# Optimization experiments

Hardware: AMD Instinct MI355X
Metric: run time of the kernel (lower is better)

Reference implementation:

```python
import jax, jax.numpy as jnp
from jax import lax
import numpy as np

B, C, H, W = 8, 256, 64, 64
STRIDE, NH = 2, 8
ED_QK, ED_V = 64, 256  # embed_dim//ratio (divisible by heads), embed_dim
HQ, WQ = H // STRIDE, W // STRIDE
L = HQ * WQ


def conv2d(x, w, b, stride=1, pad=0):
    y = lax.conv_general_dilated(x, w, (stride, stride), ((pad, pad), (pad, pad)),
                                 dimension_numbers=('NCHW', 'OIHW', 'NCHW'))
    return y + b[None, :, None, None]


def setup_inputs() -> dict:
    key = jax.random.key(0)
    ks = jax.random.split(key, 24)
    s = 0.05
    f32 = jnp.float32
    inp = {
        'qkv_pos': jax.random.normal(ks[0], (B, C, H, W), f32),
        'qkv_cha': jax.random.normal(ks[1], (B, C, H, W), f32),
        # POS branch params (standard convs)
        'Wq_pos': jax.random.normal(ks[2], (ED_QK, C, 2, 2), f32) * s,
        'bq_pos': jax.random.normal(ks[3], (ED_QK,), f32) * s,
        'Wk_pos': jax.random.normal(ks[4], (ED_QK, C, 2, 2), f32) * s,
        'bk_pos': jax.random.normal(ks[5], (ED_QK,), f32) * s,
        'Wv_pos': jax.random.normal(ks[6], (ED_V, C, 2, 2), f32) * s,
        'bv_pos': jax.random.normal(ks[7], (ED_V,), f32) * s,
        'Wo_pos': jax.random.normal(ks[8], (C, ED_V, 3, 3), f32) * s,
        'bo_pos': jax.random.normal(ks[9], (C,), f32) * s,
        'gamma_pos': jnp.full((1,), 0.5, f32),
        # CHA branch params (grouped convs, groups=C, 1 in-ch -> NH out-ch per group)
        'Wq_cha': jax.random.normal(ks[10], (C, NH, 2, 2), f32) * s,
        'bq_cha': jax.random.normal(ks[11], (C, NH), f32) * s,
        'Wk_cha': jax.random.normal(ks[12], (C, NH, 2, 2), f32) * s,
        'bk_cha': jax.random.normal(ks[13], (C, NH), f32) * s,
        'Wv_cha': jax.random.normal(ks[14], (C, NH, 2, 2), f32) * s,
        'bv_cha': jax.random.normal(ks[15], (C, NH), f32) * s,
        # grouped ConvTranspose2d (groups=C, NH in-ch per group -> 1 out-ch), k=s=2
        'Wt_cha': jax.random.normal(ks[16], (C, NH, 2, 2), f32) * s,
        'bt_cha': jax.random.normal(ks[17], (C,), f32) * s,
        'gamma_cha': jnp.full((1,), 0.5, f32),
        # fusion conv: concat -> 2C in, C out, 3x3
        'Wf': jax.random.normal(ks[18], (C, 2 * C, 3, 3), f32) * s,
        'bf': jax.random.normal(ks[19], (C,), f32) * s,
    }
    return inp


def _gproj(x, w, b):
    # grouped conv with kernel==stride==2, 1 in-ch per group -> NH out-ch per group
    xp = x.reshape(B, C, HQ, STRIDE, WQ, STRIDE)
    y = jnp.einsum('bgikjl,ghkl->bghij', xp, w) + b[None, :, :, None, None]
    # channel order c = g*NH + h (torch grouped-conv layout); torch then reshapes
    # the flat C*NH channels into (NH, C) -> same as a direct reshape here
    return y.reshape(B, NH, C, L)


def reference(qkv_pos, qkv_cha, Wq_pos, bq_pos, Wk_pos, bk_pos, Wv_pos, bv_pos,
              Wo_pos, bo_pos, gamma_pos, Wq_cha, bq_cha, Wk_cha, bk_cha,
              Wv_cha, bv_cha, Wt_cha, bt_cha, gamma_cha, Wf, bf):
    hd = ED_QK // NH
    # ---- POS (spatial) attention ----
    qp = conv2d(qkv_pos, Wq_pos, bq_pos, STRIDE).reshape(B, NH, hd, L).transpose(0, 1, 3, 2)
    kp = conv2d(qkv_pos, Wk_pos, bk_pos, STRIDE).reshape(B, NH, hd, L).transpose(0, 1, 3, 2)
    vp = conv2d(qkv_pos, Wv_pos, bv_pos, STRIDE).reshape(B, NH, ED_V // NH, L).transpose(0, 1, 3, 2)
    attn_p = jax.nn.softmax(jnp.einsum('bhqd,bhkd->bhqk', qp, kp) * (hd ** -0.5), axis=-1)
    op = jnp.einsum('bhqk,bhkd->bhqd', attn_p, vp).transpose(0, 1, 3, 2).reshape(B, ED_V, HQ, WQ)
    op = conv2d(op, Wo_pos, bo_pos, 1, 1)
    op = jax.image.resize(op, (B, C, H, W), 'bilinear')  # Upsample(align_corners=False)
    out_pos = qkv_pos + op * gamma_pos
    # ---- CHA (channel) attention ----
    qc = _gproj(qkv_cha, Wq_cha, bq_cha)  # [B,NH,C,L]
    kc = _gproj(qkv_cha, Wk_cha, bk_cha)
    vc = _gproj(qkv_cha, Wv_cha, bv_cha)
    attn_c = jax.nn.softmax(jnp.einsum('bhcl,bhdl->bhcd', qc, kc) * (L ** -0.5), axis=-1)
    oc = jnp.einsum('bhcd,bhdl->bhcl', attn_c, vc)  # [B,NH,C,L]
    # flat channel c = h*C + g; grouped ConvTranspose2d groups by c//NH -> reshape (C,NH)
    ocg = oc.reshape(B, C, NH, HQ, WQ)
    oc = jnp.einsum('bgipq,gikl->bgpkql', ocg, Wt_cha).reshape(B, C, H, W) + bt_cha[None, :, None, None]
    out_cha = qkv_cha + oc * gamma_cha
    # ---- fusion: concat (slices are full since slides=0) + 3x3 conv ----
    out = jnp.concatenate([out_pos, out_cha], axis=1)
    return conv2d(out, Wf, bf, 1, 1)
```

## Files before the change

### kernel.cpp

```cpp
#include <hip/hip_runtime.h>
#include <math.h>


typedef __attribute__((ext_vector_type(8))) short bf16x8;
typedef __attribute__((ext_vector_type(4))) float f32x4;

__device__ __forceinline__ ushort f2bf(float f) {
  union { float f; unsigned u; } v; v.f = f;
  unsigned r = (v.u + 0x7FFFu + ((v.u >> 16) & 1u)) >> 16;
  return (ushort)r;
}

__global__ __launch_bounds__(256) void k_prep_all(
    const float* __restrict__ Wf, const float* __restrict__ Wo,
    const float* __restrict__ Wq, const float* __restrict__ Wk,
    const float* __restrict__ Wv,
    ushort* __restrict__ Wpf9, ushort* __restrict__ Wpo9,
    ushort* __restrict__ Wqkvp)
{
  const int i = blockIdx.x * 256 + threadIdx.x;
  if (i < 1179648) {
    const int t = i / 131072;
    const int r = i - t * 131072;
    const int oc = r >> 9, c = r & 511;
    Wpf9[i] = f2bf(Wf[((size_t)oc * 512 + c) * 9 + t]);
  } else if (i < 1179648 + 589824) {
    const int j = i - 1179648;
    const int t = j / 65536;
    const int r = j - t * 65536;
    const int oc = r >> 8, c = r & 255;
    Wpo9[j] = f2bf(Wo[((size_t)oc * 256 + c) * 9 + t]);
  } else {
    const int j = i - 1769472;
    const int o = j >> 10, k = j & 1023;
    float v;
    if (o < 64)       v = Wq[(size_t)o * 1024 + k];
    else if (o < 128) v = Wk[(size_t)(o - 64) * 1024 + k];
    else              v = Wv[(size_t)(o - 128) * 1024 + k];
    Wqkvp[j] = f2bf(v);
  }
}

__global__ __launch_bounds__(256) void k_zero_init(
    ushort* __restrict__ fused, ushort* __restrict__ op_pad,
    ushort* __restrict__ Qb)
{
  const int t = blockIdx.x * 256 + threadIdx.x;
  uint4 z = {0u, 0u, 0u, 0u};
  if (t < 133120) {
    const int e = t & 63;
    const int pi = (t >> 6) % 260;
    const int b = t / 16640;
    int y, x;
    if (pi < 66)       { y = 0;            x = pi; }
    else if (pi < 132) { y = 65;           x = pi - 66; }
    else if (pi < 196) { y = pi - 132 + 1; x = 0; }
    else               { y = pi - 196 + 1; x = 65; }
    *(uint4*)(fused + ((size_t)b * 4356 + y * 66 + x) * 512 + e * 8) = z;
  } else if (t < 133120 + 33792) {
    const int j = t - 133120;
    const int e = j & 31;
    const int pi = (j >> 5) % 132;
    const int b = j / 4224;
    int y, x;
    if (pi < 34)       { y = 0;            x = pi; }
    else if (pi < 68)  { y = 33;           x = pi - 34; }
    else if (pi < 100) { y = pi - 68 + 1;  x = 0; }
    else               { y = pi - 100 + 1; x = 33; }
    *(uint4*)(op_pad + ((size_t)b * 1156 + y * 34 + x) * 256 + e * 8) = z;
  } else {
    const int j = t - 166912;
    *(uint4*)(Qb + (size_t)j * 8) = z;
  }
}

__global__ __launch_bounds__(256) void k_pack_pos(
    const float* __restrict__ x, ushort* __restrict__ Ap)
{
  const int t = blockIdx.x * 256 + threadIdx.x;
  const int j4 = t & 7;
  const int i  = (t >> 3) & 31;
  const int c  = (t >> 8) & 255;
  const int b  = t >> 16;
  const float* xb = x + (((size_t)b * 256 + c) << 12) + (2 * i) * 64 + 8 * j4;
  union { float4 v[2]; float f[8]; } r0, r1;
  r0.v[0] = *(const float4*)(xb);
  r0.v[1] = *(const float4*)(xb + 4);
  r1.v[0] = *(const float4*)(xb + 64);
  r1.v[1] = *(const float4*)(xb + 68);
  #pragma unroll
  for (int jj = 0; jj < 4; ++jj) {
    const int l = i * 32 + j4 * 4 + jj;
    union { ushort u[4]; uint2 d; } pk;
    pk.u[0] = f2bf(r0.f[2 * jj]);
    pk.u[1] = f2bf(r0.f[2 * jj + 1]);
    pk.u[2] = f2bf(r1.f[2 * jj]);
    pk.u[3] = f2bf(r1.f[2 * jj + 1]);
    *(uint2*)(Ap + ((((size_t)b << 10) + l) << 10) + c * 4) = pk.d;
  }
}

__global__ __launch_bounds__(256) void k_pos_qkv_mfma(
    const ushort* __restrict__ Ap, const ushort* __restrict__ Wqkv,
    const float* __restrict__ bq, const float* __restrict__ bk,
    const float* __restrict__ bv,
    ushort* __restrict__ Qb, ushort* __restrict__ Kb, ushort* __restrict__ Vtb)
{
  const int n0 = blockIdx.x * 128, oc0 = blockIdx.y * 128, b = blockIdx.z;
  const int tid = threadIdx.x, lane = tid & 63, w = tid >> 6;
  __shared__ ushort As[128][32], Bs[128][32];
  const ushort* Abw = Wqkv + (size_t)oc0 * 1024;
  const ushort* Bb  = Ap + (((size_t)b << 10) + n0) * 1024;
  const int wr = w >> 1, wc = w & 1;
  f32x4 acc[4][4];
  #pragma unroll
  for (int mi = 0; mi < 4; ++mi)
    #pragma unroll
    for (int ni = 0; ni < 4; ++ni) {
      f32x4 z = {0.f, 0.f, 0.f, 0.f};
      acc[mi][ni] = z;
    }
  for (int kc = 0; kc < 1024; kc += 32) {
    __syncthreads();
    #pragma unroll
    for (int q = 0; q < 2; ++q) {
      int idx = w * 128 + q * 64 + lane;
      int row = idx >> 2, seg = idx & 3;
      const ushort* srcA = Abw + (size_t)row * 1024 + kc + seg * 8;
      const ushort* srcB = Bb + (size_t)row * 1024 + kc + seg * 8;
      char* dstA = (char*)&As[0][0] + w * 2048 + q * 1024;
      char* dstB = (char*)&Bs[0][0] + w * 2048 + q * 1024;
      __builtin_amdgcn_global_load_lds(
          (const __attribute__((address_space(1))) unsigned*)srcA,
          (__attribute__((address_space(3))) unsigned*)dstA, 16, 0, 0);
      __builtin_amdgcn_global_load_lds(
          (const __attribute__((address_space(1))) unsigned*)srcB,
          (__attribute__((address_space(3))) unsigned*)dstB, 16, 0, 0);
    }
    __syncthreads();
    bf16x8 af[4], bfv[4];
    #pragma unroll
    for (int mi = 0; mi < 4; ++mi)
      af[mi] = *(const bf16x8*)&As[wr * 64 + mi * 16 + (lane & 15)][(lane >> 4) * 8];
    #pragma unroll
    for (int ni = 0; ni < 4; ++ni)
      bfv[ni] = *(const bf16x8*)&Bs[wc * 64 + ni * 16 + (lane & 15)][(lane >> 4) * 8];
    #pragma unroll
    for (int mi = 0; mi < 4; ++mi)
      #pragma unroll
      for (int ni = 0; ni < 4; ++ni)
        acc[mi][ni] = __builtin_amdgcn_mfma_f32_16x16x32_bf16(
            af[mi], bfv[ni], acc[mi][ni], 0, 0, 0);
  }
  #pragma unroll
  for (int mi = 0; mi < 4; ++mi) {
    const int oc = oc0 + wr * 64 + mi * 16 + (lane >> 4) * 4;
    if (oc >= 384) continue;
    if (oc < 64) {
      const int hh = oc >> 3, e = oc & 7;
      float4 bb = *(const float4*)(bq + oc);
      #pragma unroll
      for (int ni = 0; ni < 4; ++ni) {
        const int l = n0 + wc * 64 + ni * 16 + (lane & 15);
        union { ushort u[4]; uint2 d; } pk;
        pk.u[0] = f2bf((acc[mi][ni][0] + bb.x) * 0.35355339059327373f);
        pk.u[1] = f2bf((acc[mi][ni][1] + bb.y) * 0.35355339059327373f);
        pk.u[2] = f2bf((acc[mi][ni][2] + bb.z) * 0.35355339059327373f);
        pk.u[3] = f2bf((acc[mi][ni][3] + bb.w) * 0.35355339059327373f);
        *(uint2*)(Qb + (((((size_t)b * 8 + hh) << 10) + l) << 5) + e) = pk.d;
      }
    } else if (oc < 128) {
      const int o2 = oc - 64, hh = o2 >> 3, e = o2 & 7;
      float4 bb = *(const float4*)(bk + o2);
      #pragma unroll
      for (int ni = 0; ni < 4; ++ni) {
        const int l = n0 + wc * 64 + ni * 16 + (lane & 15);
        union { ushort u[4]; uint2 d; } pk;
        pk.u[0] = f2bf(acc[mi][ni][0] + bb.x);
        pk.u[1] = f2bf(acc[mi][ni][1] + bb.y);
        pk.u[2] = f2bf(acc[mi][ni][2] + bb.z);
        pk.u[3] = f2bf(acc[mi][ni][3] + bb.w);
        *(uint2*)(Kb + (((((size_t)b * 8 + hh) << 10) + l) << 5) + e) = pk.d;
      }
    } else {
      const int o2 = oc - 128, hh = o2 >> 5, dd = o2 & 31;
      float4 bb = *(const float4*)(bv + o2);
      #pragma unroll
      for (int ni = 0; ni < 4; ++ni) {
        const int l = n0 + wc * 64 + ni * 16 + (lane & 15);
        ushort* vb = Vtb + ((((size_t)b * 8 + hh) * 32 + dd) << 10) + l;
        vb[0]      = f2bf(acc[mi][ni][0] + bb.x);
        vb[1024]   = f2bf(acc[mi][ni][1] + bb.y);
        vb[2048]   = f2bf(acc[mi][ni][2] + bb.z);
        vb[3072]   = f2bf(acc[mi][ni][3] + bb.w);
      }
    }
  }
}

__global__ __launch_bounds__(256) void k_pos_flash(
    const ushort* __restrict__ Qb, const ushort* __restrict__ Kb,
    const ushort* __restrict__ Vtb, ushort* __restrict__ op_pad)
{
  const int qt = blockIdx.x, h = blockIdx.y, b = blockIdx.z;
  const int bh = b * 8 + h;
  const int tid = threadIdx.x, lane = tid & 63, wq = tid >> 6;
  const int c = lane & 15, g = lane >> 4;
  __shared__ __align__(16) ushort Ps[4][32][72];
  const int qbase = qt * 128 + wq * 32;
  bf16x8 qf[2];
  #pragma unroll
  for (int nt = 0; nt < 2; ++nt)
    qf[nt] = *(const bf16x8*)(Qb + (((size_t)bh << 10) + qbase + nt * 16 + c) * 32 + g * 8);
  f32x4 o[2][2];
  #pragma unroll
  for (int mt = 0; mt < 2; ++mt)
    #pragma unroll
    for (int nt = 0; nt < 2; ++nt) {
      f32x4 z = {0.f, 0.f, 0.f, 0.f};
      o[mt][nt] = z;
    }
  float m[2] = {-1e30f, -1e30f}, l[2] = {0.f, 0.f};
  const ushort* Kbh = Kb + ((size_t)bh << 15);
  const ushort* Vbh = Vtb + ((size_t)bh << 15);

  for (int kt = 0; kt < 16; ++kt) {
    const int kb0 = kt * 64;
    bf16x8 kf[4];
    #pragma unroll
    for (int mt = 0; mt < 4; ++mt)
      kf[mt] = *(const bf16x8*)(Kbh + (size_t)(kb0 + mt * 16 + c) * 32 + g * 8);
    f32x4 s[4][2];
    #pragma unroll
    for (int mt = 0; mt < 4; ++mt)
      #pragma unroll
      for (int nt = 0; nt < 2; ++nt) {
        f32x4 z = {0.f, 0.f, 0.f, 0.f};
        s[mt][nt] = __builtin_amdgcn_mfma_f32_16x16x32_bf16(kf[mt], qf[nt], z, 0, 0, 0);
      }
    #pragma unroll
    for (int nt = 0; nt < 2; ++nt) {
      float tmax = -1e30f;
      #pragma unroll
      for (int mt = 0; mt < 4; ++mt)
        #pragma unroll
        for (int r = 0; r < 4; ++r)
          tmax = fmaxf(tmax, s[mt][nt][r]);
      tmax = fmaxf(tmax, __shfl_xor(tmax, 16, 64));
      tmax = fmaxf(tmax, __shfl_xor(tmax, 32, 64));
      const float mn = fmaxf(m[nt], tmax);
      const float alpha = __expf(m[nt] - mn);
      m[nt] = mn;
      float rs = 0.f;
      #pragma unroll
      for (int mt = 0; mt < 4; ++mt) {
        union { ushort u[4]; uint2 d; } pk;
        #pragma unroll
        for (int r = 0; r < 4; ++r) {
          float p = __expf(s[mt][nt][r] - mn);
          rs += p;
          pk.u[r] = f2bf(p);
        }
        *(uint2*)&Ps[wq][nt * 16 + c][mt * 16 + g * 4] = pk.d;
      }
      rs += __shfl_xor(rs, 16, 64);
      rs += __shfl_xor(rs, 32, 64);
      l[nt] = l[nt] * alpha + rs;
      #pragma unroll
      for (int mt = 0; mt < 2; ++mt)
        #pragma unroll
        for (int r = 0; r < 4; ++r)
          o[mt][nt][r] *= alpha;
    }
    #pragma unroll
    for (int kc = 0; kc < 2; ++kc) {
      bf16x8 vf[2], pf[2];
      #pragma unroll
      for (int mt = 0; mt < 2; ++mt)
        vf[mt] = *(const bf16x8*)(Vbh + (size_t)(mt * 16 + c) * 1024 + kb0 + kc * 32 + g * 8);
      #pragma unroll
      for (int nt = 0; nt < 2; ++nt)
        pf[nt] = *(const bf16x8*)&Ps[wq][nt * 16 + c][kc * 32 + g * 8];
      #pragma unroll
      for (int mt = 0; mt < 2; ++mt)
        #pragma unroll
        for (int nt = 0; nt < 2; ++nt)
          o[mt][nt] = __builtin_amdgcn_mfma_f32_16x16x32_bf16(vf[mt], pf[nt], o[mt][nt], 0, 0, 0);
    }
  }
  #pragma unroll
  for (int nt = 0; nt < 2; ++nt) {
    const float linv = 1.f / l[nt];
    const int q = qbase + nt * 16 + c;
    const int y = q >> 5, x = q & 31;
    ushort* dst = op_pad + ((size_t)b * 1156 + (y + 1) * 34 + (x + 1)) * 256 + h * 32;
    #pragma unroll
    for (int mt = 0; mt < 2; ++mt) {
      union { ushort u[4]; uint2 d; } pk;
      #pragma unroll
      for (int r = 0; r < 4; ++r)
        pk.u[r] = f2bf(o[mt][nt][r] * linv);
      *(uint2*)(dst + mt * 16 + g * 4) = pk.d;
    }
  }
}

template <int CIN, int S, int PW, int OUT_NHWC, int BN>
__global__ __launch_bounds__(256) void k_conv9_mfma(
    const ushort* __restrict__ in, const ushort* __restrict__ W9,
    const float* __restrict__ bias, float* __restrict__ out)
{
  constexpr int BQ = BN / 64;
  constexpr int NI = BN / 32;
  const int n0 = blockIdx.x * BN, oc0 = blockIdx.y * 128, b = blockIdx.z;
  const int tid = threadIdx.x, lane = tid & 63, w = tid >> 6;
  __shared__ ushort As[128][32], Bs[BN][32];
  const int wr = w >> 1, wc = w & 1;
  f32x4 acc[4][NI];
  #pragma unroll
  for (int mi = 0; mi < 4; ++mi)
    #pragma unroll
    for (int ni = 0; ni < NI; ++ni) {
      f32x4 z = {0.f, 0.f, 0.f, 0.f};
      acc[mi][ni] = z;
    }
  int rowqA[2], segqA[2];
  #pragma unroll
  for (int q = 0; q < 2; ++q) {
    int idx = w * 128 + q * 64 + lane;
    rowqA[q] = idx >> 2;
    segqA[q] = (idx & 3) * 8;
  }
  int rowqB[BQ], segqB[BQ], basep[BQ];
  #pragma unroll
  for (int q = 0; q < BQ; ++q) {
    int idx = (BQ == 2) ? (w * 128 + q * 64 + lane) : tid;
    rowqB[q] = idx >> 2;
    segqB[q] = (idx & 3) * 8;
    int n = n0 + rowqB[q];
    int y = n / S, x = n % S;
    basep[q] = y * PW + x;
  }
  const ushort* inb = in + (size_t)b * (PW * PW) * CIN;

  for (int t = 0; t < 9; ++t) {
    const int offp = (t / 3) * PW + (t % 3);
    const ushort* wt = W9 + (size_t)t * 256 * CIN;
    for (int kc = 0; kc < CIN; kc += 32) {
      __syncthreads();
      #pragma unroll
      for (int q = 0; q < 2; ++q) {
        const ushort* srcA = wt + (size_t)(oc0 + rowqA[q]) * CIN + kc + segqA[q];
        char* dstA = (char*)&As[0][0] + w * 2048 + q * 1024;
        __builtin_amdgcn_global_load_lds(
            (const __attribute__((address_space(1))) unsigned*)srcA,
            (__attribute__((address_space(3))) unsigned*)dstA, 16, 0, 0);
      }
      #pragma unroll
      for (int q = 0; q < BQ; ++q) {
        const ushort* srcB = inb + (size_t)(basep[q] + offp) * CIN + kc + segqB[q];
        char* dstB = (char*)&Bs[0][0] + w * (BQ * 1024) + q * 1024;
        __builtin_amdgcn_global_load_lds(
            (const __attribute__((address_space(1))) unsigned*)srcB,
            (__attribute__((address_space(3))) unsigned*)dstB, 16, 0, 0);
      }
      __syncthreads();
      bf16x8 af[4], bfv[NI];
      #pragma unroll
      for (int mi = 0; mi < 4; ++mi)
        af[mi] = *(const bf16x8*)&As[wr * 64 + mi * 16 + (lane & 15)][(lane >> 4) * 8];
      #pragma unroll
      for (int ni = 0; ni < NI; ++ni)
        bfv[ni] = *(const bf16x8*)&Bs[wc * (BN / 2) + ni * 16 + (lane & 15)][(lane >> 4) * 8];
      #pragma unroll
      for (int mi = 0; mi < 4; ++mi)
        #pragma unroll
        for (int ni = 0; ni < NI; ++ni)
          acc[mi][ni] = __builtin_amdgcn_mfma_f32_16x16x32_bf16(
              af[mi], bfv[ni], acc[mi][ni], 0, 0, 0);
    }
  }
  if (OUT_NHWC) {
    float* outb = out + (size_t)b * (S * S) * 256;
    #pragma unroll
    for (int mi = 0; mi < 4; ++mi) {
      const int oc = oc0 + wr * 64 + mi * 16 + (lane >> 4) * 4;
      float4 bb = *(const float4*)(bias + oc);
      #pragma unroll
      for (int ni = 0; ni < NI; ++ni) {
        const int n = n0 + wc * (BN / 2) + ni * 16 + (lane & 15);
        float4 v;
        v.x = acc[mi][ni][0] + bb.x;
        v.y = acc[mi][ni][1] + bb.y;
        v.z = acc[mi][ni][2] + bb.z;
        v.w = acc[mi][ni][3] + bb.w;
        *(float4*)(outb + (size_t)n * 256 + oc) = v;
      }
    }
  } else {
    float* outb = out + (size_t)b * 256 * (S * S);
    #pragma unroll
    for (int mi = 0; mi < 4; ++mi) {
      #pragma unroll
      for (int r = 0; r < 4; ++r) {
        int oc = oc0 + wr * 64 + mi * 16 + (lane >> 4) * 4 + r;
        float bb = bias[oc];
        #pragma unroll
        for (int ni = 0; ni < NI; ++ni) {
          int n = n0 + wc * (BN / 2) + ni * 16 + (lane & 15);
          outb[(size_t)oc * (S * S) + n] = acc[mi][ni][r] + bb;
        }
      }
    }
  }
}

#define STAGE_CONV(s_, bi_)                                                    \
  {                                                                            \
    const int t_ = (s_) >> 3, kc_ = ((s_) & 7) << 6;                           \
    const ushort* wt_ = W9 + t_ * 131072 + kc_;                                \
    const ushort* ib_ = inb + ((t_ / 3) * 66 + (t_ % 3)) * 512 + kc_;          \
    _Pragma("unroll")                                                          \
    for (int q_ = 0; q_ < 2; ++q_) {                                           \
      __builtin_amdgcn_global_load_lds(                                        \
          (const __attribute__((address_space(1))) unsigned*)(wt_ + aInv[q_]), \
          (__attribute__((address_space(3))) unsigned*)                        \
              ((char*)lds + (bi_) * 16384 + (w * 16 + q_ * 8) * 128),          \
          16, 0, 0);                                                           \
    }                                                                          \
    _Pragma("unroll")                                                          \
    for (int q_ = 0; q_ < 4; ++q_) {                                           \
      __builtin_amdgcn_global_load_lds(                                        \
          (const __attribute__((address_space(1))) unsigned*)(ib_ + bInv[q_]), \
          (__attribute__((address_space(3))) unsigned*)                        \
              ((char*)lds + 49152 + (bi_) * 32768 + (w * 32 + q_ * 8) * 128),  \
          16, 0, 0);                                                           \
    }                                                                          \
  }

#define READ_FRAGS(rb_, AF_, BF_)                                              \
  {                                                                            \
    const ushort* As_ = lds + (rb_) * 8192 + (wm * 64 + c) * 64;               \
    const ushort* Bs_ = lds + 24576 + (rb_) * 16384 + (wn * 64 + c) * 64;      \
    _Pragma("unroll")                                                          \
    for (int mi_ = 0; mi_ < 4; ++mi_) {                                        \
      AF_[mi_][0] = *(const bf16x8*)(As_ + mi_ * 1024 + okh0);                 \
      AF_[mi_][1] = *(const bf16x8*)(As_ + mi_ * 1024 + okh1);                 \
    }                                                                          \
    _Pragma("unroll")                                                          \
    for (int ni_ = 0; ni_ < 4; ++ni_) {                                        \
      BF_[ni_][0] = *(const bf16x8*)(Bs_ + ni_ * 1024 + okh0);                 \
      BF_[ni_][1] = *(const bf16x8*)(Bs_ + ni_ * 1024 + okh1);                 \
    }                                                                          \
  }

#define MFMA_SET(AF_, BF_)                                                     \
  {                                                                            \
    __builtin_amdgcn_s_setprio(1);                                             \
    _Pragma("unroll")                                                          \
    for (int mi_ = 0; mi_ < 4; ++mi_)                                          \
      _Pragma("unroll")                                                        \
      for (int ni_ = 0; ni_ < 4; ++ni_) {                                      \
        acc[mi_][ni_] = __builtin_amdgcn_mfma_f32_16x16x32_bf16(               \
            AF_[mi_][0], BF_[ni_][0], acc[mi_][ni_], 0, 0, 0);                 \
        acc[mi_][ni_] = __builtin_amdgcn_mfma_f32_16x16x32_bf16(               \
            AF_[mi_][1], BF_[ni_][1], acc[mi_][ni_], 0, 0, 0);                 \
      }                                                                        \
    __builtin_amdgcn_s_setprio(0);                                             \
  }

#define PHASE_END(vm_)                                                         \
  {                                                                            \
    asm volatile("s_waitcnt lgkmcnt(0)" ::: "memory");                         \
    asm volatile("s_waitcnt vmcnt(" #vm_ ")" ::: "memory");                    \
    __builtin_amdgcn_sched_barrier(0);                                         \
    __builtin_amdgcn_s_barrier();                                              \
  }

__global__ __launch_bounds__(512, 2) void k_conv9_pipe(
    const ushort* __restrict__ in, const ushort* __restrict__ W9,
    const float* __restrict__ bias, float* __restrict__ out)
{
  const int n0 = blockIdx.x * 256, oc0 = blockIdx.y * 128, b = blockIdx.z;
  const int tid = threadIdx.x, lane = tid & 63, w = tid >> 6;
  const int wm = w >> 2, wn = w & 3;
  const int g = lane >> 4, c = lane & 15;
  __shared__ __align__(16) ushort lds[73728];
  const ushort* inb = in + (size_t)b * 4356 * 512;

  const int l8 = lane >> 3, lx = lane & 7;
  int aInv[2], bInv[4];
  #pragma unroll
  for (int q = 0; q < 2; ++q) {
    const int row = w * 16 + q * 8 + l8;
    const int cx = (((lx << 4) ^ ((row & 7) << 4)) >> 1);
    aInv[q] = (oc0 + row) * 512 + cx;
  }
  #pragma unroll
  for (int q = 0; q < 4; ++q) {
    const int row = w * 32 + q * 8 + l8;
    const int n = n0 + row;
    const int y = n >> 6, x = n & 63;
    const int cx = (((lx << 4) ^ ((row & 7) << 4)) >> 1);
    bInv[q] = (y * 66 + x) * 512 + cx;
  }

  const int sx = (c & 7) << 3;
  const int okh0 = (g * 8) ^ sx;
  const int okh1 = (32 + g * 8) ^ sx;

  f32x4 acc[4][4];
  #pragma unroll
  for (int mi = 0; mi < 4; ++mi)
    #pragma unroll
    for (int ni = 0; ni < 4; ++ni) {
      f32x4 z = {0.f, 0.f, 0.f, 0.f};
      acc[mi][ni] = z;
    }

  bf16x8 afE[4][2], bfE[4][2], afO[4][2], bfO[4][2];

  STAGE_CONV(0, 0);
  STAGE_CONV(1, 1);
  STAGE_CONV(2, 2);
  asm volatile("s_waitcnt vmcnt(12)" ::: "memory");
  __builtin_amdgcn_sched_barrier(0);
  __builtin_amdgcn_s_barrier();
  READ_FRAGS(0, afE, bfE);
  PHASE_END(6);

  int rb = 1;
  for (int p = 0; p < 68; p += 2) {
    READ_FRAGS(rb, afO, bfO);
    { int sb = rb + 2; if (sb >= 3) sb -= 3; STAGE_CONV(p + 3, sb); }
    MFMA_SET(afE, bfE);
    PHASE_END(6);
    ++rb; if (rb == 3) rb = 0;
    READ_FRAGS(rb, afE, bfE);
    { int sb = rb + 2; if (sb >= 3) sb -= 3; STAGE_CONV(p + 4, sb); }
    MFMA_SET(afO, bfO);
    PHASE_END(6);
    ++rb; if (rb == 3) rb = 0;
  }
  READ_FRAGS(rb, afO, bfO);
  { int sb = rb + 2; if (sb >= 3) sb -= 3; STAGE_CONV(71, sb); }
  MFMA_SET(afE, bfE);
  PHASE_END(6);
  ++rb; if (rb == 3) rb = 0;
  READ_FRAGS(rb, afE, bfE);
  MFMA_SET(afO, bfO);
  PHASE_END(0);
  ++rb; if (rb == 3) rb = 0;
  READ_FRAGS(rb, afO, bfO);
  MFMA_SET(afE, bfE);
  asm volatile("s_waitcnt lgkmcnt(0)" ::: "memory");
  __builtin_amdgcn_sched_barrier(0);
  __builtin_amdgcn_s_barrier();
  MFMA_SET(afO, bfO);

  float* outb = out + (size_t)b * 1048576;
  #pragma unroll
  for (int mi = 0; mi < 4; ++mi) {
    const int oc = oc0 + wm * 64 + mi * 16 + g * 4;
    float4 bb = *(const float4*)(bias + oc);
    #pragma unroll
    for (int ni = 0; ni < 4; ++ni) {
      const int n = n0 + wn * 64 + ni * 16 + c;
      outb[(size_t)(oc + 0) * 4096 + n] = acc[mi][ni][0] + bb.x;
      outb[(size_t)(oc + 1) * 4096 + n] = acc[mi][ni][1] + bb.y;
      outb[(size_t)(oc + 2) * 4096 + n] = acc[mi][ni][2] + bb.z;
      outb[(size_t)(oc + 3) * 4096 + n] = acc[mi][ni][3] + bb.w;
    }
  }
}

__global__ __launch_bounds__(256) void k_upsample_nhwc(
    const float* __restrict__ xpos, const float* __restrict__ opc,
    const float* __restrict__ gamma, ushort* __restrict__ fused)
{
  const int t = blockIdx.x * 256 + threadIdx.x;
  const int c = (t & 63) * 4;
  const int pix = (t >> 6) & 4095;
  const int b = t >> 18;
  const int y = pix >> 6, xx = pix & 63;
  const int my = y >> 1;
  const int y0 = (y & 1) ? my : my - 1;
  const float fy = (y & 1) ? 0.25f : 0.75f;
  const int mx = xx >> 1;
  const int x0 = (xx & 1) ? mx : mx - 1;
  const float fx = (xx & 1) ? 0.25f : 0.75f;
  const int y0c = max(y0, 0), y1c = min(y0 + 1, 31);
  const int x0c = max(x0, 0), x1c = min(x0 + 1, 31);
  const float* base = opc + (size_t)b * 1024 * 256 + c;
  float4 v00 = *(const float4*)(base + (size_t)(y0c * 32 + x0c) * 256);
  float4 v01 = *(const float4*)(base + (size_t)(y0c * 32 + x1c) * 256);
  float4 v10 = *(const float4*)(base + (size_t)(y1c * 32 + x0c) * 256);
  float4 v11 = *(const float4*)(base + (size_t)(y1c * 32 + x1c) * 256);
  const float w00 = (1.f - fy) * (1.f - fx), w01 = (1.f - fy) * fx;
  const float w10 = fy * (1.f - fx), w11 = fy * fx;
  const float g = gamma[0];
  const float* xr = xpos + ((size_t)b * 256 + c) * 4096 + pix;
  union { ushort u[4]; uint2 q; } o;
  o.u[0] = f2bf(xr[0]          + g * (w00 * v00.x + w01 * v01.x + w10 * v10.x + w11 * v11.x));
  o.u[1] = f2bf(xr[4096]       + g * (w00 * v00.y + w01 * v01.y + w10 * v10.y + w11 * v11.y));
  o.u[2] = f2bf(xr[2 * 4096]   + g * (w00 * v00.z + w01 * v01.z + w10 * v10.z + w11 * v11.z));
  o.u[3] = f2bf(xr[3 * 4096]   + g * (w00 * v00.w + w01 * v01.w + w10 * v10.w + w11 * v11.w));
  *(uint2*)(fused + ((size_t)b * 4356 + (y + 1) * 66 + (xx + 1)) * 512 + c) = o.q;
}

__global__ __launch_bounds__(256) void k_cha_proj(
    const float* __restrict__ x,
    const float* __restrict__ Wq, const float* __restrict__ bq,
    const float* __restrict__ Wk, const float* __restrict__ bk,
    const float* __restrict__ Wv, const float* __restrict__ bv,
    ushort* __restrict__ Qc, ushort* __restrict__ Kc, ushort* __restrict__ Vt)
{
  const int t = blockIdx.x * 256 + threadIdx.x;
  const int bl = t >> 16;
  const int g  = (t >> 8) & 255;
  const int lq = t & 255;
  const int i = lq >> 3, j4 = (lq & 7) << 2;
  const float* xb = x + (((size_t)bl * 256 + g) << 12) + (2 * i) * 64 + 2 * j4;
  union { float4 v[2]; float f[8]; } xr0, xr1;
  xr0.v[0] = *(const float4*)(xb);
  xr0.v[1] = *(const float4*)(xb + 4);
  xr1.v[0] = *(const float4*)(xb + 64);
  xr1.v[1] = *(const float4*)(xb + 68);
  const int bhl = bl * 8 + (g >> 5);
  const int c2b = (g & 31) * 8;
  const int l0 = i * 32 + j4;
  #pragma unroll
  for (int h = 0; h < 8; ++h) {
    float4 w4 = *(const float4*)(Wq + g * 32 + h * 4);
    float bb = bq[g * 8 + h];
    union { ushort u[4]; uint2 q; } o;
    #pragma unroll
    for (int jj = 0; jj < 4; ++jj) {
      float v = xr0.f[2 * jj] * w4.x + xr0.f[2 * jj + 1] * w4.y
              + xr1.f[2 * jj] * w4.z + xr1.f[2 * jj + 1] * w4.w + bb;
      o.u[jj] = f2bf(v * 0.03125f);
    }
    *(uint2*)(Qc + (((size_t)bhl * 256 + c2b + h) << 10) + l0) = o.q;
  }
  #pragma unroll
  for (int h = 0; h < 8; ++h) {
    float4 w4 = *(const float4*)(Wk + g * 32 + h * 4);
    float bb = bk[g * 8 + h];
    union { ushort u[4]; uint2 q; } o;
    #pragma unroll
    for (int jj = 0; jj < 4; ++jj) {
      float v = xr0.f[2 * jj] * w4.x + xr0.f[2 * jj + 1] * w4.y
              + xr1.f[2 * jj] * w4.z + xr1.f[2 * jj + 1] * w4.w + bb;
      o.u[jj] = f2bf(v);
    }
    *(uint2*)(Kc + (((size_t)bhl * 256 + c2b + h) << 10) + l0) = o.q;
  }
  ushort vo[4][8];
  #pragma unroll
  for (int h = 0; h < 8; ++h) {
    float4 w4 = *(const float4*)(Wv + g * 32 + h * 4);
    float bb = bv[g * 8 + h];
    #pragma unroll
    for (int jj = 0; jj < 4; ++jj) {
      float v = xr0.f[2 * jj] * w4.x + xr0.f[2 * jj + 1] * w4.y
              + xr1.f[2 * jj] * w4.z + xr1.f[2 * jj + 1] * w4.w + bb;
      vo[jj][h] = f2bf(v);
    }
  }
  #pragma unroll
  for (int jj = 0; jj < 4; ++jj)
    *(uint4*)(Vt + ((size_t)bhl << 18) + (size_t)(l0 + jj) * 256 + c2b) =
        *(uint4*)&vo[jj][0];
}

__global__ __launch_bounds__(256) void k_cha_scores_mfma(
    const ushort* __restrict__ Qc, const ushort* __restrict__ Kc,
    float* __restrict__ S)
{
  const int c0 = blockIdx.x * 128, d0 = blockIdx.y * 64, bhl = blockIdx.z;
  const int tid = threadIdx.x, lane = tid & 63, w = tid >> 6;
  __shared__ ushort As[128][32], Bs[64][32];
  const ushort* Ab = Qc + ((size_t)bhl * 256 + c0) * 1024;
  const ushort* Bb = Kc + ((size_t)bhl * 256 + d0) * 1024;
  const int wr = w >> 1, wc = w & 1;
  f32x4 acc[4][2];
  #pragma unroll
  for (int mi = 0; mi < 4; ++mi)
    #pragma unroll
    for (int ni = 0; ni < 2; ++ni) {
      f32x4 z = {0.f, 0.f, 0.f, 0.f};
      acc[mi][ni] = z;
    }
  for (int kc = 0; kc < 1024; kc += 32) {
    __syncthreads();
    #pragma unroll
    for (int q = 0; q < 2; ++q) {
      int idx = w * 128 + q * 64 + lane;
      int row = idx >> 2, seg = idx & 3;
      const ushort* srcA = Ab + (size_t)row * 1024 + kc + seg * 8;
      char* dstA = (char*)&As[0][0] + w * 2048 + q * 1024;
      __builtin_amdgcn_global_load_lds(
          (const __attribute__((address_space(1))) unsigned*)srcA,
          (__attribute__((address_space(3))) unsigned*)dstA, 16, 0, 0);
    }
    {
      int idx = tid;
      int row = idx >> 2, seg = idx & 3;
      const ushort* srcB = Bb + (size_t)row * 1024 + kc + seg * 8;
      char* dstB = (char*)&Bs[0][0] + w * 1024;
      __builtin_amdgcn_global_load_lds(
          (const __attribute__((address_space(1))) unsigned*)srcB,
          (__attribute__((address_space(3))) unsigned*)dstB, 16, 0, 0);
    }
    __syncthreads();
    bf16x8 af[4], bfv[2];
    #pragma unroll
    for (int mi = 0; mi < 4; ++mi)
      af[mi] = *(const bf16x8*)&As[wr * 64 + mi * 16 + (lane & 15)][(lane >> 4) * 8];
    #pragma unroll
    for (int ni = 0; ni < 2; ++ni)
      bfv[ni] = *(const bf16x8*)&Bs[wc * 32 + ni * 16 + (lane & 15)][(lane >> 4) * 8];
    #pragma unroll
    for (int mi = 0; mi < 4; ++mi)
      #pragma unroll
      for (int ni = 0; ni < 2; ++ni)
        acc[mi][ni] = __builtin_amdgcn_mfma_f32_16x16x32_bf16(
            af[mi], bfv[ni], acc[mi][ni], 0, 0, 0);
  }
  float* Sb = S + ((size_t)bhl << 16);
  #pragma unroll
  for (int mi = 0; mi < 4; ++mi)
    #pragma unroll
    for (int r = 0; r < 4; ++r) {
      int c = c0 + wr * 64 + mi * 16 + (lane >> 4) * 4 + r;
      #pragma unroll
      for (int ni = 0; ni < 2; ++ni) {
        int d = d0 + wc * 32 + ni * 16 + (lane & 15);
        Sb[(size_t)c * 256 + d] = acc[mi][ni][r];
      }
    }
}

__global__ __launch_bounds__(256) void k_softmax_p(
    const float* __restrict__ S, ushort* __restrict__ P)
{
  const int row = blockIdx.x * 4 + (threadIdx.x >> 6);
  const int lane = threadIdx.x & 63;
  const float* r = S + (size_t)row * 256;
  float4 v = *(const float4*)(r + lane * 4);
  float m = fmaxf(fmaxf(v.x, v.y), fmaxf(v.z, v.w));
  #pragma unroll
  for (int off = 32; off; off >>= 1) m = fmaxf(m, __shfl_xor(m, off, 64));
  v.x = __expf(v.x - m); v.y = __expf(v.y - m);
  v.z = __expf(v.z - m); v.w = __expf(v.w - m);
  float s = v.x + v.y + v.z + v.w;
  #pragma unroll
  for (int off = 32; off; off >>= 1) s += __shfl_xor(s, off, 64);
  const float inv = 1.f / s;
  union { ushort u[4]; uint2 q; } o;
  o.u[0] = f2bf(v.x * inv); o.u[1] = f2bf(v.y * inv);
  o.u[2] = f2bf(v.z * inv); o.u[3] = f2bf(v.w * inv);
  *(uint2*)(P + (size_t)row * 256 + lane * 4) = o.q;
}

__global__ __launch_bounds__(256) void k_cha_pv(
    const ushort* __restrict__ P, const ushort* __restrict__ Vt,
    const float* __restrict__ x,
    const float* __restrict__ Wt, const float* __restrict__ bt,
    const float* __restrict__ gamma, ushort* __restrict__ fused, int bbase)
{
  const int n0 = blockIdx.x * 128, c0 = blockIdx.y * 128, bhl = blockIdx.z;
  const int b = bbase + (bhl >> 3), h = bhl & 7;
  const int tid = threadIdx.x, lane = tid & 63, w = tid >> 6;
  __shared__ ushort As[128][32], Bs[128][32];
  __shared__ ushort Ot[512][16];
  __shared__ float wt_s[16][32];
  __shared__ float bt_s[16];
  const int gp_base = h * 32 + (c0 >> 3);
  {
    int e = tid;
    wt_s[e >> 5][e & 31] = Wt[(size_t)gp_base * 32 + e];
    e += 256;
    wt_s[e >> 5][e & 31] = Wt[(size_t)gp_base * 32 + e];
    if (tid < 16) bt_s[tid] = bt[gp_base + tid];
  }
  const ushort* Ab = P + (((size_t)bhl << 8) + c0) * 256;
  const ushort* Bb = Vt + ((size_t)bhl << 18) + (size_t)n0 * 256;
  const int wr = w >> 1, wc = w & 1;
  f32x4 acc[4][4];
  #pragma unroll
  for (int mi = 0; mi < 4; ++mi)
    #pragma unroll
    for (int ni = 0; ni < 4; ++ni) {
      f32x4 z = {0.f, 0.f, 0.f, 0.f};
      acc[mi][ni] = z;
    }
  for (int kc = 0; kc < 256; kc += 32) {
    __syncthreads();
    #pragma unroll
    for (int q = 0; q < 2; ++q) {
      int idx = w * 128 + q * 64 + lane;
      int row = idx >> 2, seg = idx & 3;
      const ushort* srcA = Ab + (size_t)row * 256 + kc + seg * 8;
      const ushort* srcB = Bb + (size_t)row * 256 + kc + seg * 8;
      char* dstA = (char*)&As[0][0] + w * 2048 + q * 1024;
      char* dstB = (char*)&Bs[0][0] + w * 2048 + q * 1024;
      __builtin_amdgcn_global_load_lds(
          (const __attribute__((address_space(1))) unsigned*)srcA,
          (__attribute__((address_space(3))) unsigned*)dstA, 16, 0, 0);
      __builtin_amdgcn_global_load_lds(
          (const __attribute__((address_space(1))) unsigned*)srcB,
          (__attribute__((address_space(3))) unsigned*)dstB, 16, 0, 0);
    }
    __syncthreads();
    bf16x8 af[4], bfv[4];
    #pragma unroll
    for (int mi = 0; mi < 4; ++mi)
      af[mi] = *(const bf16x8*)&As[wr * 64 + mi * 16 + (lane & 15)][(lane >> 4) * 8];
    #pragma unroll
    for (int ni = 0; ni < 4; ++ni)
      bfv[ni] = *(const bf16x8*)&Bs[wc * 64 + ni * 16 + (lane & 15)][(lane >> 4) * 8];
    #pragma unroll
    for (int mi = 0; mi < 4; ++mi)
      #pragma unroll
      for (int ni = 0; ni < 4; ++ni)
        acc[mi][ni] = __builtin_amdgcn_mfma_f32_16x16x32_bf16(
            af[mi], bfv[ni], acc[mi][ni], 0, 0, 0);
  }
  const float gm = gamma[0];
  const int col = lane & 15, q = lane >> 4;
  #pragma unroll
  for (int mi = 0; mi < 4; ++mi) {
    const int gloc = wr * 8 + mi * 2 + (q >> 1);
    const int gp = gp_base + gloc;
    const float btv = bt_s[gloc];
    #pragma unroll
    for (int ni = 0; ni < 4; ++ni) {
      float pa[4] = {0.f, 0.f, 0.f, 0.f};
      #pragma unroll
      for (int r = 0; r < 4; ++r) {
        const int i2 = (q & 1) * 4 + r;
        const float a = acc[mi][ni][r];
        pa[0] += a * wt_s[gloc][i2 * 4 + 0];
        pa[1] += a * wt_s[gloc][i2 * 4 + 1];
        pa[2] += a * wt_s[gloc][i2 * 4 + 2];
        pa[3] += a * wt_s[gloc][i2 * 4 + 3];
      }
      float v0 = pa[0] + __shfl_xor(pa[0], 16, 64);
      float v1 = pa[1] + __shfl_xor(pa[1], 16, 64);
      float v2 = pa[2] + __shfl_xor(pa[2], 16, 64);
      float v3 = pa[3] + __shfl_xor(pa[3], 16, 64);
      const int lloc = wc * 64 + ni * 16 + col;
      const int l = n0 + lloc;
      const int p = l >> 5, j = l & 31;
      const int y = 2 * p + (q & 1);
      const float va = (q & 1) ? v2 : v0;
      const float vb = (q & 1) ? v3 : v1;
      const float* xc = x + (((size_t)b * 256 + gp) << 12) + (y << 6) + 2 * j;
      const int lp = (lloc << 2) + (q & 1) * 2;
      Ot[lp][gloc]     = f2bf(xc[0] + gm * (va + btv));
      Ot[lp + 1][gloc] = f2bf(xc[1] + gm * (vb + btv));
    }
  }
  __syncthreads();
  #pragma unroll
  for (int pp2 = 0; pp2 < 2; ++pp2) {
    const int pixl = tid * 2 + pp2;
    const int lloc = pixl >> 2;
    const int l = n0 + lloc;
    const int p = l >> 5, j = l & 31;
    const int yy = 2 * p + ((pixl >> 1) & 1) + 1;
    const int xx = 2 * j + (pixl & 1) + 1;
    const uint4* src = (const uint4*)&Ot[pixl][0];
    uint4* dst = (uint4*)(fused + ((size_t)b * 4356 + yy * 66 + xx) * 512 + 256 + gp_base);
    dst[0] = src[0];
    dst[1] = src[1];
  }
}

extern "C" void kernel_launch(void* const* d_in, const int* in_sizes, int n_in,
                              void* d_out, int out_size, void* d_ws, size_t ws_size,
                              hipStream_t stream)
{
  (void)in_sizes; (void)n_in; (void)out_size; (void)ws_size;
  const float* qkv_pos   = (const float*)d_in[0];
  const float* qkv_cha   = (const float*)d_in[1];
  const float* Wq_pos    = (const float*)d_in[2];
  const float* bq_pos    = (const float*)d_in[3];
  const float* Wk_pos    = (const float*)d_in[4];
  const float* bk_pos    = (const float*)d_in[5];
  const float* Wv_pos    = (const float*)d_in[6];
  const float* bv_pos    = (const float*)d_in[7];
  const float* Wo_pos    = (const float*)d_in[8];
  const float* bo_pos    = (const float*)d_in[9];
  const float* gamma_pos = (const float*)d_in[10];
  const float* Wq_cha    = (const float*)d_in[11];
  const float* bq_cha    = (const float*)d_in[12];
  const float* Wk_cha    = (const float*)d_in[13];
  const float* bk_cha    = (const float*)d_in[14];
  const float* Wv_cha    = (const float*)d_in[15];
  const float* bv_cha    = (const float*)d_in[16];
  const float* Wt_cha    = (const float*)d_in[17];
  const float* bt_cha    = (const float*)d_in[18];
  const float* gamma_cha = (const float*)d_in[19];
  const float* Wf        = (const float*)d_in[20];
  const float* bf        = (const float*)d_in[21];
  float* out = (float*)d_out;

  float* ws = (float*)d_ws;
  ushort* Wpf9    = (ushort*)ws;
  ushort* Wpo9    = (ushort*)(ws + 589824);
  ushort* Qb      = (ushort*)(ws + 884736);
  ushort* Kb      = (ushort*)(ws + 1933312);
  ushort* Vtb     = (ushort*)(ws + 2981888);
  ushort* op_pad  = (ushort*)(ws + 4030464);
  float*  op_conv = ws + 5214208;
  ushort* Ap      = (ushort*)(ws + 7311360);
  ushort* qcb     = (ushort*)(ws + 884736);
  ushort* kcb     = (ushort*)(ws + 5079040);
  ushort* vcT     = (ushort*)(ws + 9273344);
  float*  attn_c  = ws + 13467648;
  ushort* Pb      = (ushort*)(ws + 15564800);
  ushort* fusedb  = (ushort*)(ws + 16613376);
  ushort* Wqkvp   = (ushort*)(ws + 25534464);

  k_zero_init<<<dim3(1676), 256, 0, stream>>>(fusedb, op_pad, Qb);
  k_prep_all<<<dim3(8448), 256, 0, stream>>>(Wf, Wo_pos, Wq_pos, Wk_pos,
      Wv_pos, Wpf9, Wpo9, Wqkvp);
  k_pack_pos<<<dim3(2048), 256, 0, stream>>>(qkv_pos, Ap);
  k_pos_qkv_mfma<<<dim3(8, 3, 8), 256, 0, stream>>>(Ap, Wqkvp,
      bq_pos, bk_pos, bv_pos, Qb, Kb, Vtb);
  k_pos_flash<<<dim3(8, 8, 8), 256, 0, stream>>>(Qb, Kb, Vtb, op_pad);
  k_conv9_mfma<256, 32, 34, 1, 64><<<dim3(16, 2, 8), 256, 0, stream>>>(
      op_pad, Wpo9, bo_pos, op_conv);
  k_upsample_nhwc<<<dim3(8192), 256, 0, stream>>>(qkv_pos, op_conv, gamma_pos, fusedb);
  for (int half = 0; half < 2; ++half) {
    const float* xh = qkv_cha + (size_t)half * 4 * 256 * 4096;
    k_cha_proj<<<dim3(1024), 256, 0, stream>>>(xh, Wq_cha, bq_cha,
        Wk_cha, bk_cha, Wv_cha, bv_cha, qcb, kcb, vcT);
    k_cha_scores_mfma<<<dim3(2, 4, 32), 256, 0, stream>>>(qcb, kcb, attn_c);
    k_softmax_p<<<dim3(2048), 256, 0, stream>>>(attn_c, Pb);
    k_cha_pv<<<dim3(8, 2, 32), 256, 0, stream>>>(Pb, vcT, qkv_cha,
        Wt_cha, bt_cha, gamma_cha, fusedb, half * 4);
  }
  k_conv9_pipe<<<dim3(16, 2, 8), 512, 0, stream>>>(fusedb, Wpf9, bf, out);
}
```

Measured before the change: 520.0 us.

## Merge init kernels and stage pack/upsample transposes through shared memory

Folds the zero-init and weight-prep kernels into one launch to save a kernel launch. Rewrites k_pack_pos and k_upsample_nhwc to load NCHW rows with coalesced float4 reads into padded LDS tiles, then emit NHWC/bf16 output from LDS, replacing the strided per-channel global reads. This targets uncoalesced global traffic in layout-transpose kernels, at the cost of more LDS use per block and fewer, larger blocks.

```diff
diff --git a/kernel.cpp b/kernel.cpp
--- a/kernel.cpp
+++ b/kernel.cpp
@@ -11,39 +11,14 @@
   return (ushort)r;
 }
 
-__global__ __launch_bounds__(256) void k_prep_all(
+__global__ __launch_bounds__(256) void k_init_all(
+    ushort* __restrict__ fused, ushort* __restrict__ op_pad,
+    ushort* __restrict__ Qb,
     const float* __restrict__ Wf, const float* __restrict__ Wo,
     const float* __restrict__ Wq, const float* __restrict__ Wk,
     const float* __restrict__ Wv,
     ushort* __restrict__ Wpf9, ushort* __restrict__ Wpo9,
     ushort* __restrict__ Wqkvp)
-{
-  const int i = blockIdx.x * 256 + threadIdx.x;
-  if (i < 1179648) {
-    const int t = i / 131072;
-    const int r = i - t * 131072;
-    const int oc = r >> 9, c = r & 511;
-    Wpf9[i] = f2bf(Wf[((size_t)oc * 512 + c) * 9 + t]);
-  } else if (i < 1179648 + 589824) {
-    const int j = i - 1179648;
-    const int t = j / 65536;
-    const int r = j - t * 65536;
-    const int oc = r >> 8, c = r & 255;
-    Wpo9[j] = f2bf(Wo[((size_t)oc * 256 + c) * 9 + t]);
-  } else {
-    const int j = i - 1769472;
-    const int o = j >> 10, k = j & 1023;
-    float v;
-    if (o < 64)       v = Wq[(size_t)o * 1024 + k];
-    else if (o < 128) v = Wk[(size_t)(o - 64) * 1024 + k];
-    else              v = Wv[(size_t)(o - 128) * 1024 + k];
-    Wqkvp[j] = f2bf(v);
-  }
-}
-
-__global__ __launch_bounds__(256) void k_zero_init(
-    ushort* __restrict__ fused, ushort* __restrict__ op_pad,
-    ushort* __restrict__ Qb)
 {
   const int t = blockIdx.x * 256 + threadIdx.x;
   uint4 z = {0u, 0u, 0u, 0u};
@@ -57,7 +32,7 @@
     else if (pi < 196) { y = pi - 132 + 1; x = 0; }
     else               { y = pi - 196 + 1; x = 65; }
     *(uint4*)(fused + ((size_t)b * 4356 + y * 66 + x) * 512 + e * 8) = z;
-  } else if (t < 133120 + 33792) {
+  } else if (t < 166912) {
     const int j = t - 133120;
     const int e = j & 31;
     const int pi = (j >> 5) % 132;
@@ -68,35 +43,60 @@
     else if (pi < 100) { y = pi - 68 + 1;  x = 0; }
     else               { y = pi - 100 + 1; x = 33; }
     *(uint4*)(op_pad + ((size_t)b * 1156 + y * 34 + x) * 256 + e * 8) = z;
-  } else {
+  } else if (t < 429056) {
     const int j = t - 166912;
     *(uint4*)(Qb + (size_t)j * 8) = z;
+  } else {
+    const int i = t - 429056;
+    if (i < 1179648) {
+      const int tt = i / 131072;
+      const int r = i - tt * 131072;
+      const int oc = r >> 9, c = r & 511;
+      Wpf9[i] = f2bf(Wf[((size_t)oc * 512 + c) * 9 + tt]);
+    } else if (i < 1769472) {
+      const int j = i - 1179648;
+      const int tt = j / 65536;
+      const int r = j - tt * 65536;
+      const int oc = r >> 8, c = r & 255;
+      Wpo9[j] = f2bf(Wo[((size_t)oc * 256 + c) * 9 + tt]);
+    } else {
+      const int j = i - 1769472;
+      const int o = j >> 10, k = j & 1023;
+      float v;
+      if (o < 64)       v = Wq[(size_t)o * 1024 + k];
+      else if (o < 128) v = Wk[(size_t)(o - 64) * 1024 + k];
+      else              v = Wv[(size_t)(o - 128) * 1024 + k];
+      Wqkvp[j] = f2bf(v);
+    }
   }
 }
 
 __global__ __launch_bounds__(256) void k_pack_pos(
     const float* __restrict__ x, ushort* __restrict__ Ap)
 {
-  const int t = blockIdx.x * 256 + threadIdx.x;
-  const int j4 = t & 7;
-  const int i  = (t >> 3) & 31;
-  const int c  = (t >> 8) & 255;
-  const int b  = t >> 16;
-  const float* xb = x + (((size_t)b * 256 + c) << 12) + (2 * i) * 64 + 8 * j4;
-  union { float4 v[2]; float f[8]; } r0, r1;
-  r0.v[0] = *(const float4*)(xb);
-  r0.v[1] = *(const float4*)(xb + 4);
-  r1.v[0] = *(const float4*)(xb + 64);
-  r1.v[1] = *(const float4*)(xb + 68);
-  #pragma unroll
-  for (int jj = 0; jj < 4; ++jj) {
-    const int l = i * 32 + j4 * 4 + jj;
+  const int i = blockIdx.x, b = blockIdx.y;
+  const int tid = threadIdx.x;
+  __shared__ ushort xs[256][132];
+  #pragma unroll 4
+  for (int it = 0; it < 32; ++it) {
+    const int slot = it * 256 + tid;
+    const int px4 = slot & 15, r = (slot >> 4) & 1, c = slot >> 5;
+    float4 v = *(const float4*)(x + (((size_t)b * 256 + c) << 12)
+                                + (2 * i + r) * 64 + px4 * 4);
     union { ushort u[4]; uint2 d; } pk;
-    pk.u[0] = f2bf(r0.f[2 * jj]);
-    pk.u[1] = f2bf(r0.f[2 * jj + 1]);
-    pk.u[2] = f2bf(r1.f[2 * jj]);
-    pk.u[3] = f2bf(r1.f[2 * jj + 1]);
-    *(uint2*)(Ap + ((((size_t)b << 10) + l) << 10) + c * 4) = pk.d;
+    pk.u[0] = f2bf(v.x); pk.u[1] = f2bf(v.y);
+    pk.u[2] = f2bf(v.z); pk.u[3] = f2bf(v.w);
+    *(uint2*)&xs[c][r * 64 + px4 * 4] = pk.d;
+  }
+  __syncthreads();
+  ushort* dst = Ap + ((((size_t)b << 10) + i * 32) << 10);
+  const int c = tid;
+  #pragma unroll 4
+  for (int j = 0; j < 32; ++j) {
+    uint2 o;
+    o.x = *(const uint*)&xs[c][2 * j];
+    o.y = *(const uint*)&xs[c][64 + 2 * j];
+    *(uint2*)(dst + (size_t)j * 1024 + c * 4) = o;
   }
 }
 
@@ -578,34 +578,63 @@
     const float* __restrict__ xpos, const float* __restrict__ opc,
     const float* __restrict__ gamma, ushort* __restrict__ fused)
 {
-  const int t = blockIdx.x * 256 + threadIdx.x;
-  const int c = (t & 63) * 4;
-  const int pix = (t >> 6) & 4095;
-  const int b = t >> 18;
-  const int y = pix >> 6, xx = pix & 63;
+  const int y = blockIdx.x, h0 = blockIdx.y * 128, b = blockIdx.z;
+  const int tid = threadIdx.x;
+  __shared__ float xs[128 * 65];
+  __shared__ float os[64 * 132];
   const int my = y >> 1;
   const int y0 = (y & 1) ? my : my - 1;
   const float fy = (y & 1) ? 0.25f : 0.75f;
-  const int mx = xx >> 1;
-  const int x0 = (xx & 1) ? mx : mx - 1;
-  const float fx = (xx & 1) ? 0.25f : 0.75f;
   const int y0c = max(y0, 0), y1c = min(y0 + 1, 31);
-  const int x0c = max(x0, 0), x1c = min(x0 + 1, 31);
-  const float* base = opc + (size_t)b * 1024 * 256 + c;
-  float4 v00 = *(const float4*)(base + (size_t)(y0c * 32 + x0c) * 256);
-  float4 v01 = *(const float4*)(base + (size_t)(y0c * 32 + x1c) * 256);
-  float4 v10 = *(const float4*)(base + (size_t)(y1c * 32 + x0c) * 256);
-  float4 v11 = *(const float4*)(base + (size_t)(y1c * 32 + x1c) * 256);
-  const float w00 = (1.f - fy) * (1.f - fx), w01 = (1.f - fy) * fx;
-  const float w10 = fy * (1.f - fx), w11 = fy * fx;
+  #pragma unroll
+  for (int it = 0; it < 8; ++it) {
+    const int slot = it * 256 + tid;
+    const int px4 = slot & 15, cp = slot >> 4;
+    float4 v = *(const float4*)(xpos + (((size_t)b * 256 + h0 + cp) << 12)
+                                + y * 64 + px4 * 4);
+    xs[cp * 65 + px4 * 4 + 0] = v.x;
+    xs[cp * 65 + px4 * 4 + 1] = v.y;
+    xs[cp * 65 + px4 * 4 + 2] = v.z;
+    xs[cp * 65 + px4 * 4 + 3] = v.w;
+  }
+  #pragma unroll
+  for (int it = 0; it < 8; ++it) {
+    const int slot = it * 256 + tid;
+    const int cc4 = slot & 31, pxe = slot >> 5;
+    const int row = (pxe < 32) ? y0c : y1c;
+    const int col = pxe & 31;
+    float4 v = *(const float4*)(opc + ((size_t)b * 1024 + row * 32 + col) * 256
+                                + h0 + cc4 * 4);
+    *(float4*)&os[pxe * 132 + cc4 * 4] = v;
+  }
+  __syncthreads();
   const float g = gamma[0];
-  const float* xr = xpos + ((size_t)b * 256 + c) * 4096 + pix;
-  union { ushort u[4]; uint2 q; } o;
-  o.u[0] = f2bf(xr[0]          + g * (w00 * v00.x + w01 * v01.x + w10 * v10.x + w11 * v11.x));
-  o.u[1] = f2bf(xr[4096]       + g * (w00 * v00.y + w01 * v01.y + w10 * v10.y + w11 * v11.y));
-  o.u[2] = f2bf(xr[2 * 4096]   + g * (w00 * v00.z + w01 * v01.z + w10 * v10.z + w11 * v11.z));
-  o.u[3] = f2bf(xr[3 * 4096]   + g * (w00 * v00.w + w01 * v01.w + w10 * v10.w + w11 * v11.w));
-  *(uint2*)(fused + ((size_t)b * 4356 + (y + 1) * 66 + (xx + 1)) * 512 + c) = o.q;
+  #pragma unroll
+  for (int it = 0; it < 8; ++it) {
+    const int xx = it * 8 + (tid >> 5);
+    const int c4 = tid & 31;
+    const int mx = xx >> 1;
+    const int x0 = (xx & 1) ? mx : mx - 1;
+    const float fx = (xx & 1) ? 0.25f : 0.75f;
+    const int x0c = max(x0, 0), x1c = min(x0 + 1, 31);
+    float4 v00 = *(const float4*)&os[x0c * 132 + c4 * 4];
+    float4 v01 = *(const float4*)&os[x1c * 132 + c4 * 4];
+    float4 v10 = *(const float4*)&os[(32 + x0c) * 132 + c4 * 4];
+    float4 v11 = *(const float4*)&os[(32 + x1c) * 132 + c4 * 4];
+    const float w00 = (1.f - fy) * (1.f - fx), w01 = (1.f - fy) * fx;
+    const float w10 = fy * (1.f - fx), w11 = fy * fx;
+    union { ushort u[4]; uint2 q; } o;
+    o.u[0] = f2bf(xs[(c4 * 4 + 0) * 65 + xx]
+                  + g * (w00 * v00.x + w01 * v01.x + w10 * v10.x + w11 * v11.x));
+    o.u[1] = f2bf(xs[(c4 * 4 + 1) * 65 + xx]
+                  + g * (w00 * v00.y + w01 * v01.y + w10 * v10.y + w11 * v11.y));
+    o.u[2] = f2bf(xs[(c4 * 4 + 2) * 65 + xx]
+                  + g * (w00 * v00.z + w01 * v01.z + w10 * v10.z + w11 * v11.z));
+    o.u[3] = f2bf(xs[(c4 * 4 + 3) * 65 + xx]
+                  + g * (w00 * v00.w + w01 * v01.w + w10 * v10.w + w11 * v11.w));
+    *(uint2*)(fused + ((size_t)b * 4356 + (y + 1) * 66 + (xx + 1)) * 512
+              + h0 + c4 * 4) = o.q;
+  }
 }
 
 __global__ __launch_bounds__(256) void k_cha_proj(
@@ -924,16 +953,16 @@
   ushort* fusedb  = (ushort*)(ws + 16613376);
   ushort* Wqkvp   = (ushort*)(ws + 25534464);
 
-  k_zero_init<<<dim3(1676), 256, 0, stream>>>(fusedb, op_pad, Qb);
-  k_prep_all<<<dim3(8448), 256, 0, stream>>>(Wf, Wo_pos, Wq_pos, Wk_pos,
-      Wv_pos, Wpf9, Wpo9, Wqkvp);
-  k_pack_pos<<<dim3(2048), 256, 0, stream>>>(qkv_pos, Ap);
+  k_init_all<<<dim3(10124), 256, 0, stream>>>(fusedb, op_pad, Qb,
+      Wf, Wo_pos, Wq_pos, Wk_pos, Wv_pos, Wpf9, Wpo9, Wqkvp);
+  k_pack_pos<<<dim3(32, 8), 256, 0, stream>>>(qkv_pos, Ap);
   k_pos_qkv_mfma<<<dim3(8, 3, 8), 256, 0, stream>>>(Ap, Wqkvp,
       bq_pos, bk_pos, bv_pos, Qb, Kb, Vtb);
   k_pos_flash<<<dim3(8, 8, 8), 256, 0, stream>>>(Qb, Kb, Vtb, op_pad);
   k_conv9_mfma<256, 32, 34, 1, 64><<<dim3(16, 2, 8), 256, 0, stream>>>(
       op_pad, Wpo9, bo_pos, op_conv);
-  k_upsample_nhwc<<<dim3(8192), 256, 0, stream>>>(qkv_pos, op_conv, gamma_pos, fusedb);
+  k_upsample_nhwc<<<dim3(64, 2, 8), 256, 0, stream>>>(qkv_pos, op_conv,
+      gamma_pos, fusedb);
   for (int half = 0; half < 2; ++half) {
     const float* xh = qkv_cha + (size_t)half * 4 * 256 * 4096;
     k_cha_proj<<<dim3(1024), 256, 0, stream>>>(xh, Wq_cha, bq_cha,
```

Result: faster. 459.4 us (-11.7%).
